# Optimization experiments

Measured on AMD Instinct MI355X. Metric: run time of the kernel, lower is better.

The kernel has to match this reference:

```python
import jax, jax.numpy as jnp
import numpy as np

D_MODEL = 1024
N_HEADS = 16
HEAD_DIM = D_MODEL // N_HEADS


def setup_inputs() -> dict:
    key = jax.random.key(0)
    ks = jax.random.split(key, 11)
    B, S = 2, 2048
    s = 1.0 / np.sqrt(D_MODEL)
    return {
        "query": jax.random.normal(ks[0], (B, S, D_MODEL), jnp.float32),
        "key": jax.random.normal(ks[1], (B, S, D_MODEL), jnp.float32),
        "value": jax.random.normal(ks[2], (B, S, D_MODEL), jnp.float32),
        "Wq": jax.random.normal(ks[3], (D_MODEL, D_MODEL), jnp.float32) * s,
        "bq": jnp.zeros((D_MODEL,), jnp.float32),
        "Wk": jax.random.normal(ks[4], (D_MODEL, D_MODEL), jnp.float32) * s,
        "bk": jnp.zeros((D_MODEL,), jnp.float32),
        "Wv": jax.random.normal(ks[5], (D_MODEL, D_MODEL), jnp.float32) * s,
        "bv": jnp.zeros((D_MODEL,), jnp.float32),
        "Wo": jax.random.normal(ks[6], (D_MODEL, D_MODEL), jnp.float32) * s,
        "bo": jnp.zeros((D_MODEL,), jnp.float32),
    }


def reference(query, key, value, Wq, bq, Wk, bk, Wv, bv, Wo, bo):
    B, S, _ = query.shape
    H, Dh = N_HEADS, HEAD_DIM
    scale = jnp.sqrt(jnp.asarray(Dh, query.dtype))
    # projections (torch Linear: x @ W.T + b)
    Q = (query @ Wq.T + bq).reshape(B, S, H, Dh).transpose(0, 2, 1, 3)  # [B,H,S,Dh]
    K = (key @ Wk.T + bk).reshape(B, S, H, Dh).transpose(0, 2, 1, 3)
    V = (value @ Wv.T + bv).reshape(B, S, H, Dh).transpose(0, 2, 1, 3)
    # full score matrix, matching the naive formulation
    energy = jnp.einsum("bhqd,bhkd->bhqk", Q, K) / scale  # [B,H,S,S]
    attn = jax.nn.softmax(energy, axis=-1)
    # dropout: eval mode -> identity
    out = jnp.einsum("bhqk,bhkd->bhqd", attn, V)  # [B,H,S,Dh]
    out = out.transpose(0, 2, 1, 3).reshape(B, S, H * Dh)
    return out @ Wo.T + bo
```

## Files before the change

### kernel.cpp

```cpp
#include <hip/hip_runtime.h>
#include <hip/hip_bf16.h>
#include <stdint.h>


typedef unsigned short u16;
typedef __attribute__((ext_vector_type(8))) short bf16x8;
typedef __attribute__((ext_vector_type(4))) float f32x4;

#define MFMA16 __builtin_amdgcn_mfma_f32_16x16x32_bf16
#define AS1 __attribute__((address_space(1)))
#define AS3 __attribute__((address_space(3)))

#define GM 4096
#define GN 1024
#define GK 1024
#define S_LEN 2048
#define NH 16
#define DH 64
#define KVBLK 64
#define PSTR 72

__device__ __forceinline__ u16 f2bf(float f) {
    union { float f; uint32_t u; } v; v.f = f;
    return (u16)((v.u + 0x7fffu + ((v.u >> 16) & 1u)) >> 16);
}

__device__ __forceinline__ uint32_t pack_bf16(float lo, float hi) {
    float2 t; t.x = lo; t.y = hi;
    __hip_bfloat162 h = __float22bfloat162_rn(t);
    return *(uint32_t*)&h;
}

__global__ __launch_bounds__(256) void cvt_all_kernel(
        const float* __restrict__ q, const float* __restrict__ k, const float* __restrict__ v,
        const float* __restrict__ Wq, const float* __restrict__ Wk,
        const float* __restrict__ Wv, const float* __restrict__ Wo,
        const float* __restrict__ bq,
        u16* __restrict__ qbf, u16* __restrict__ kbf, u16* __restrict__ vbf,
        u16* __restrict__ Wqb, u16* __restrict__ Wkb, u16* __restrict__ Wvb,
        u16* __restrict__ Wob, float* __restrict__ bqs, float qscale) {
    int bid = blockIdx.x;
    if (bid >= 8192) {
        int i = (bid - 8192) * 256 + (int)threadIdx.x;
        if (i < GN) bqs[i] = bq[i] * qscale;
        return;
    }
    const float* src; u16* dst; float scale = 1.f; int off;
    if      (bid < 2048) { src = q;  dst = qbf; off = bid; }
    else if (bid < 4096) { src = k;  dst = kbf; off = bid - 2048; }
    else if (bid < 6144) { src = v;  dst = vbf; off = bid - 4096; }
    else if (bid < 6656) { src = Wq; dst = Wqb; off = bid - 6144; scale = qscale; }
    else if (bid < 7168) { src = Wk; dst = Wkb; off = bid - 6656; }
    else if (bid < 7680) { src = Wv; dst = Wvb; off = bid - 7168; }
    else                 { src = Wo; dst = Wob; off = bid - 7680; }
    size_t i = (size_t)off * 256 + threadIdx.x;
    const f32x4* s = (const f32x4*)src + i * 2;
    f32x4 a = s[0], b = s[1];
    union { bf16x8 v8; u16 u[8]; } o;
    o.u[0] = f2bf(a[0] * scale); o.u[1] = f2bf(a[1] * scale);
    o.u[2] = f2bf(a[2] * scale); o.u[3] = f2bf(a[3] * scale);
    o.u[4] = f2bf(b[0] * scale); o.u[5] = f2bf(b[1] * scale);
    o.u[6] = f2bf(b[2] * scale); o.u[7] = f2bf(b[3] * scale);
    *(bf16x8*)(dst + i * 8) = o.v8;
}

template<int BK>
__device__ __forceinline__ void gemm_core(const u16* __restrict__ A,
                                          const u16* __restrict__ W,
                                          const float* __restrict__ bias,
                                          void* __restrict__ Cout, int mode,
                                          u16* As, u16* Bs,
                                          int mbase, int nbase) {
    const int t  = threadIdx.x;
    const int l  = t & 63;
    const int w  = t >> 6;
    const int wr = w >> 1, wc = w & 1;
    const int cl = l & 15, g = l >> 4;
    constexpr int CPR  = BK / 8;
    constexpr int NCH  = 128 * CPR / 256;
    constexpr int TE   = 128 * BK;

    f32x4 acc[4][4];
    f32x4 zero = {0.f, 0.f, 0.f, 0.f};
    #pragma unroll
    for (int i = 0; i < 4; ++i)
        #pragma unroll
        for (int j = 0; j < 4; ++j) acc[i][j] = zero;

    auto skey = [](int row) -> int {
        if constexpr (BK == 64) return row & 7;
        else                    return (row >> 1) & 3;
    };

    auto stage = [&](int buf, int kt) {
        #pragma unroll
        for (int r = 0; r < NCH; ++r) {
            int c = r * 256 + t;
            int row = c / CPR;
            int c8 = (c % CPR) ^ skey(row);
            __builtin_amdgcn_global_load_lds(
                (const AS1 void*)(A + (size_t)(mbase + row) * GK + kt + c8 * 8),
                (AS3 void*)(As + buf * TE + c * 8), 16, 0, 0);
            __builtin_amdgcn_global_load_lds(
                (const AS1 void*)(W + (size_t)(nbase + row) * GK + kt + c8 * 8),
                (AS3 void*)(Bs + buf * TE + c * 8), 16, 0, 0);
        }
    };

    stage(0, 0);
    __syncthreads();

    int cur = 0;
    for (int kt = 0; kt < GK; kt += BK) {
        if (kt + BK < GK) stage(cur ^ 1, kt + BK);

        const u16* Asb = As + cur * TE;
        const u16* Bsb = Bs + cur * TE;
        #pragma unroll
        for (int ks = 0; ks < BK / 32; ++ks) {
            bf16x8 af[4], bfr[4];
            #pragma unroll
            for (int mi = 0; mi < 4; ++mi) {
                int row = wr * 64 + mi * 16 + cl;
                af[mi] = *(const bf16x8*)&Asb[row * BK + ((ks * 4 + g) ^ skey(row)) * 8];
            }
            #pragma unroll
            for (int nj = 0; nj < 4; ++nj) {
                int row = wc * 64 + nj * 16 + cl;
                bfr[nj] = *(const bf16x8*)&Bsb[row * BK + ((ks * 4 + g) ^ skey(row)) * 8];
            }
            #pragma unroll
            for (int mi = 0; mi < 4; ++mi)
                #pragma unroll
                for (int nj = 0; nj < 4; ++nj)
                    acc[mi][nj] = MFMA16(af[mi], bfr[nj], acc[mi][nj], 0, 0, 0);
        }
        __syncthreads();
        cur ^= 1;
    }

    #pragma unroll
    for (int mi = 0; mi < 4; ++mi) {
        #pragma unroll
        for (int nj = 0; nj < 4; ++nj) {
            int n = nbase + wc * 64 + nj * 16 + cl;
            float bv = bias[n];
            #pragma unroll
            for (int r = 0; r < 4; ++r) {
                int m = mbase + wr * 64 + mi * 16 + g * 4 + r;
                float vv = acc[mi][nj][r] + bv;
                if (mode == 2) {
                    ((float*)Cout)[(size_t)m * GN + n] = vv;
                } else {
                    int b = m >> 11, s = m & 2047;
                    int hh = n >> 6, dh = n & 63;
                    if (mode == 0)
                        ((u16*)Cout)[(((size_t)(b * NH + hh)) * S_LEN + s) * DH + dh] = f2bf(vv);
                    else
                        ((u16*)Cout)[(((size_t)(b * NH + hh)) * DH + dh) * S_LEN + s] = f2bf(vv);
                }
            }
        }
    }
}

__global__ __launch_bounds__(256) void proj_gemm(
        const u16* __restrict__ qbf, const u16* __restrict__ kbf, const u16* __restrict__ vbf,
        const u16* __restrict__ Wqb, const u16* __restrict__ Wkb, const u16* __restrict__ Wvb,
        const float* __restrict__ bq, const float* __restrict__ bk, const float* __restrict__ bv,
        u16* __restrict__ Qb, u16* __restrict__ Kb, u16* __restrict__ Vtb) {
    __shared__ u16 As[2 * 128 * 32];
    __shared__ u16 Bs[2 * 128 * 32];
    int z = blockIdx.z;
    const u16* A   = (z == 0) ? qbf : (z == 1) ? kbf : vbf;
    const u16* W   = (z == 0) ? Wqb : (z == 1) ? Wkb : Wvb;
    const float* b = (z == 0) ? bq  : (z == 1) ? bk  : bv;
    u16* C         = (z == 0) ? Qb  : (z == 1) ? Kb  : Vtb;
    gemm_core<32>(A, W, b, (void*)C, (z == 2) ? 1 : 0, As, Bs,
                  blockIdx.y * 128, blockIdx.x * 128);
}

__global__ __launch_bounds__(256) void out_gemm(const u16* __restrict__ A,
                                                const u16* __restrict__ W,
                                                const float* __restrict__ bias,
                                                float* __restrict__ C) {
    __shared__ u16 As[2 * 128 * 64];
    __shared__ u16 Bs[2 * 128 * 64];
    int bid = blockIdx.x;
    int lid = (bid & 7) * 32 + (bid >> 3);
    int x = lid & 7, y = lid >> 3;
    gemm_core<64>(A, W, bias, (void*)C, 2, As, Bs, y * 128, x * 128);
}

__global__ __launch_bounds__(512, 4) void attn_kernel(const u16* __restrict__ Q,
                                                      const u16* __restrict__ Kb,
                                                      const u16* __restrict__ Vt,
                                                      u16* __restrict__ O) {
    __shared__ u16 Ks[3][KVBLK * 64];
    __shared__ u16 Vs[3][KVBLK * 64];
    __shared__ u16 Pl[8][16 * PSTR];

    const int t = threadIdx.x, l = t & 63, w = t >> 6;
    const int cl = l & 15, g = l >> 4;
    const int bh = blockIdx.x;
    const int b = bh >> 4, h = bh & 15;
    const int qw = blockIdx.y * 128 + w * 16;

    const u16* Qp = Q  + ((size_t)bh * S_LEN + qw) * DH;
    const u16* Kp = Kb + (size_t)bh * S_LEN * DH;
    const u16* Vp = Vt + (size_t)bh * DH * S_LEN;

    bf16x8 qf0 = *(const bf16x8*)(Qp + (size_t)cl * DH + g * 8);
    bf16x8 qf1 = *(const bf16x8*)(Qp + (size_t)cl * DH + 32 + g * 8);

    float rs = 0.f;
    f32x4 oacc[4];
    f32x4 zero = {0.f, 0.f, 0.f, 0.f};
    #pragma unroll
    for (int tt = 0; tt < 4; ++tt) oacc[tt] = zero;

    u16* P = Pl[w];

    const int srow = t >> 3;
    const int sc8  = (t & 7) ^ (srow & 7);
    const u16* Kg = Kp + (size_t)srow * DH + sc8 * 8;
    const u16* Vg = Vp + (size_t)srow * S_LEN + sc8 * 8;

    #define STAGE(buf, kvoff)                                                            \
        do {                                                                             \
            __builtin_amdgcn_global_load_lds(                                            \
                (const AS1 void*)(Kg + (size_t)(kvoff) * DH),                            \
                (AS3 void*)(&Ks[buf][0] + t * 8), 16, 0, 0);                             \
            __builtin_amdgcn_global_load_lds(                                            \
                (const AS1 void*)(Vg + (kvoff)),                                         \
                (AS3 void*)(&Vs[buf][0] + t * 8), 16, 0, 0);                             \
        } while (0)

    STAGE(0, 0);
    STAGE(1, KVBLK);
    asm volatile("s_waitcnt vmcnt(2)" ::: "memory");
    __builtin_amdgcn_s_barrier();

    const int NT = S_LEN / KVBLK;
    int cur = 0;
    for (int it = 0; it < NT; ++it) {
        if (it + 2 < NT) {
            int nb = cur + 2; if (nb >= 3) nb -= 3;
            STAGE(nb, (it + 2) * KVBLK);
        }

        const u16* Ksb = &Ks[cur][0];
        const u16* Vsb = &Vs[cur][0];

        f32x4 s[4];
        #pragma unroll
        for (int j = 0; j < 4; ++j) s[j] = zero;
        __builtin_amdgcn_s_setprio(1);
        #pragma unroll
        for (int j = 0; j < 4; ++j) {
            int row = j * 16 + cl, rx = row & 7;
            bf16x8 k0 = *(const bf16x8*)&Ksb[row * 64 + ((g)     ^ rx) * 8];
            bf16x8 k1 = *(const bf16x8*)&Ksb[row * 64 + ((4 + g) ^ rx) * 8];
            s[j] = MFMA16(k0, qf0, s[j], 0, 0, 0);
            s[j] = MFMA16(k1, qf1, s[j], 0, 0, 0);
        }
        __builtin_amdgcn_s_setprio(0);

        #pragma unroll
        for (int j = 0; j < 4; ++j) {
            float p0 = __builtin_amdgcn_exp2f(s[j][0]);
            float p1 = __builtin_amdgcn_exp2f(s[j][1]);
            float p2 = __builtin_amdgcn_exp2f(s[j][2]);
            float p3 = __builtin_amdgcn_exp2f(s[j][3]);
            rs += (p0 + p1) + (p2 + p3);
            uint2 pk;
            pk.x = pack_bf16(p0, p1);
            pk.y = pack_bf16(p2, p3);
            *(uint2*)&P[cl * PSTR + j * 16 + g * 4] = pk;
        }

        bf16x8 pf[2];
        #pragma unroll
        for (int ks = 0; ks < 2; ++ks)
            pf[ks] = *(const bf16x8*)&P[cl * PSTR + ks * 32 + g * 8];

        __builtin_amdgcn_s_setprio(1);
        #pragma unroll
        for (int tt = 0; tt < 4; ++tt) {
            int row = tt * 16 + cl, rx = row & 7;
            #pragma unroll
            for (int ks = 0; ks < 2; ++ks) {
                bf16x8 vf = *(const bf16x8*)&Vsb[row * 64 + ((ks * 4 + g) ^ rx) * 8];
                oacc[tt] = MFMA16(pf[ks], vf, oacc[tt], 0, 0, 0);
            }
        }
        __builtin_amdgcn_s_setprio(0);

        if (it + 2 < NT) {
            asm volatile("s_waitcnt vmcnt(2)\n\ts_barrier" ::: "memory");
        } else {
            asm volatile("s_waitcnt vmcnt(0)\n\ts_barrier" ::: "memory");
        }
        cur = (cur + 1 == 3) ? 0 : cur + 1;
    }
    #undef STAGE

    rs += __shfl_xor(rs, 16, 64);
    rs += __shfl_xor(rs, 32, 64);
    float rsq[4];
    #pragma unroll
    for (int r = 0; r < 4; ++r)
        rsq[r] = __shfl(rs, g * 4 + r, 64);

    #pragma unroll
    for (int tt = 0; tt < 4; ++tt) {
        #pragma unroll
        for (int r = 0; r < 4; ++r) {
            int q = qw + g * 4 + r;
            float val = oacc[tt][r] / rsq[r];
            O[((size_t)b * S_LEN + q) * GN + h * DH + tt * 16 + cl] = f2bf(val);
        }
    }
}

extern "C" void kernel_launch(void* const* d_in, const int* in_sizes, int n_in,
                              void* d_out, int out_size, void* d_ws, size_t ws_size,
                              hipStream_t stream) {
    const float* query = (const float*)d_in[0];
    const float* key   = (const float*)d_in[1];
    const float* value = (const float*)d_in[2];
    const float* Wq = (const float*)d_in[3];
    const float* bq = (const float*)d_in[4];
    const float* Wk = (const float*)d_in[5];
    const float* bk = (const float*)d_in[6];
    const float* Wv = (const float*)d_in[7];
    const float* bv = (const float*)d_in[8];
    const float* Wo = (const float*)d_in[9];
    const float* bo = (const float*)d_in[10];
    float* out = (float*)d_out;

    const float QSCALE = 0.125f * 1.4426950408889634f;

    u16* ws = (u16*)d_ws;
    const size_t MD = (size_t)GM * GN;
    const size_t WW = (size_t)GN * GK;
    u16* qbf = ws;
    u16* kbf = qbf + MD;
    u16* vbf = kbf + MD;
    u16* Wqb = vbf + MD;
    u16* Wkb = Wqb + WW;
    u16* Wvb = Wkb + WW;
    u16* Wob = Wvb + WW;
    u16* Qb  = Wob + WW;
    u16* Kbf = Qb  + MD;
    u16* Vtb = Kbf + MD;
    u16* Ob  = Vtb + MD;
    float* bqs = (float*)(Ob + MD);

    cvt_all_kernel<<<8196, 256, 0, stream>>>(query, key, value, Wq, Wk, Wv, Wo, bq,
                                             qbf, kbf, vbf, Wqb, Wkb, Wvb, Wob,
                                             bqs, QSCALE);

    dim3 gproj(GN / 128, GM / 128, 3);
    proj_gemm<<<gproj, 256, 0, stream>>>(qbf, kbf, vbf, Wqb, Wkb, Wvb,
                                         bqs, bk, bv, Qb, Kbf, Vtb);

    dim3 gattn(2 * NH, S_LEN / 128);
    attn_kernel<<<gattn, 512, 0, stream>>>(Qb, Kbf, Vtb, Ob);

    out_gemm<<<256, 256, 0, stream>>>(Ob, Wob, bo, out);
}
```

Before: 126.4 us.

## Software-pipeline attention QK^T one tile ahead and shrink out-GEMM K tile

The attention loop is restructured so the QK^T MFMAs for the next KV tile are issued before the exp/PV work of the current tile, with ping-pong score registers and K loads staged three tiles ahead and V two tiles ahead. The aim is to overlap the exp2 and LDS traffic of the softmax with matrix-core work and deepen the load pipeline. Separately, the output GEMM switches from a K-tile of 64 to 32, halving its shared memory, which may allow more resident blocks at the cost of more loop iterations. The extra live score registers may raise VGPR pressure under the 512x4 launch bound.

```diff
diff --git a/kernel.cpp b/kernel.cpp
--- a/kernel.cpp
+++ b/kernel.cpp
@@ -184,12 +184,12 @@
                                                 const u16* __restrict__ W,
                                                 const float* __restrict__ bias,
                                                 float* __restrict__ C) {
-    __shared__ u16 As[2 * 128 * 64];
-    __shared__ u16 Bs[2 * 128 * 64];
+    __shared__ u16 As[2 * 128 * 32];
+    __shared__ u16 Bs[2 * 128 * 32];
     int bid = blockIdx.x;
     int lid = (bid & 7) * 32 + (bid >> 3);
     int x = lid & 7, y = lid >> 3;
-    gemm_core<64>(A, W, bias, (void*)C, 2, As, Bs, y * 128, x * 128);
+    gemm_core<32>(A, W, bias, (void*)C, 2, As, Bs, y * 128, x * 128);
 }
 
 __global__ __launch_bounds__(512, 4) void attn_kernel(const u16* __restrict__ Q,
@@ -220,90 +220,110 @@
     for (int tt = 0; tt < 4; ++tt) oacc[tt] = zero;
 
     u16* P = Pl[w];
+    const int NT = S_LEN / KVBLK;
 
     const int srow = t >> 3;
     const int sc8  = (t & 7) ^ (srow & 7);
     const u16* Kg = Kp + (size_t)srow * DH + sc8 * 8;
     const u16* Vg = Vp + (size_t)srow * S_LEN + sc8 * 8;
 
-    #define STAGE(buf, kvoff)                                                            \
-        do {                                                                             \
-            __builtin_amdgcn_global_load_lds(                                            \
-                (const AS1 void*)(Kg + (size_t)(kvoff) * DH),                            \
-                (AS3 void*)(&Ks[buf][0] + t * 8), 16, 0, 0);                             \
-            __builtin_amdgcn_global_load_lds(                                            \
-                (const AS1 void*)(Vg + (kvoff)),                                         \
-                (AS3 void*)(&Vs[buf][0] + t * 8), 16, 0, 0);                             \
-        } while (0)
-
-    STAGE(0, 0);
-    STAGE(1, KVBLK);
+    #define STAGE_K(buf, kvoff)                                                   \
+        __builtin_amdgcn_global_load_lds(                                         \
+            (const AS1 void*)(Kg + (size_t)(kvoff) * DH),                         \
+            (AS3 void*)(&Ks[buf][0] + t * 8), 16, 0, 0)
+    #define STAGE_V(buf, kvoff)                                                   \
+        __builtin_amdgcn_global_load_lds(                                         \
+            (const AS1 void*)(Vg + (kvoff)),                                      \
+            (AS3 void*)(&Vs[buf][0] + t * 8), 16, 0, 0)
+
+    STAGE_K(0, 0);
+    STAGE_K(1, KVBLK);
+    STAGE_V(0, 0);
+    STAGE_K(2, 2 * KVBLK);
+    STAGE_V(1, KVBLK);
     asm volatile("s_waitcnt vmcnt(2)" ::: "memory");
     __builtin_amdgcn_s_barrier();
 
-    const int NT = S_LEN / KVBLK;
-    int cur = 0;
-    for (int it = 0; it < NT; ++it) {
-        if (it + 2 < NT) {
-            int nb = cur + 2; if (nb >= 3) nb -= 3;
-            STAGE(nb, (it + 2) * KVBLK);
-        }
-
-        const u16* Ksb = &Ks[cur][0];
-        const u16* Vsb = &Vs[cur][0];
-
-        f32x4 s[4];
-        #pragma unroll
-        for (int j = 0; j < 4; ++j) s[j] = zero;
-        __builtin_amdgcn_s_setprio(1);
+    f32x4 sA[4], sB[4];
+    {
+        const u16* Kn = &Ks[0][0];
         #pragma unroll
         for (int j = 0; j < 4; ++j) {
-            int row = j * 16 + cl, rx = row & 7;
-            bf16x8 k0 = *(const bf16x8*)&Ksb[row * 64 + ((g)     ^ rx) * 8];
-            bf16x8 k1 = *(const bf16x8*)&Ksb[row * 64 + ((4 + g) ^ rx) * 8];
-            s[j] = MFMA16(k0, qf0, s[j], 0, 0, 0);
-            s[j] = MFMA16(k1, qf1, s[j], 0, 0, 0);
-        }
-        __builtin_amdgcn_s_setprio(0);
-
-        #pragma unroll
-        for (int j = 0; j < 4; ++j) {
-            float p0 = __builtin_amdgcn_exp2f(s[j][0]);
-            float p1 = __builtin_amdgcn_exp2f(s[j][1]);
-            float p2 = __builtin_amdgcn_exp2f(s[j][2]);
-            float p3 = __builtin_amdgcn_exp2f(s[j][3]);
-            rs += (p0 + p1) + (p2 + p3);
-            uint2 pk;
-            pk.x = pack_bf16(p0, p1);
-            pk.y = pack_bf16(p2, p3);
-            *(uint2*)&P[cl * PSTR + j * 16 + g * 4] = pk;
-        }
-
-        bf16x8 pf[2];
-        #pragma unroll
-        for (int ks = 0; ks < 2; ++ks)
-            pf[ks] = *(const bf16x8*)&P[cl * PSTR + ks * 32 + g * 8];
-
-        __builtin_amdgcn_s_setprio(1);
-        #pragma unroll
-        for (int tt = 0; tt < 4; ++tt) {
-            int row = tt * 16 + cl, rx = row & 7;
-            #pragma unroll
-            for (int ks = 0; ks < 2; ++ks) {
-                bf16x8 vf = *(const bf16x8*)&Vsb[row * 64 + ((ks * 4 + g) ^ rx) * 8];
-                oacc[tt] = MFMA16(pf[ks], vf, oacc[tt], 0, 0, 0);
-            }
-        }
-        __builtin_amdgcn_s_setprio(0);
-
-        if (it + 2 < NT) {
-            asm volatile("s_waitcnt vmcnt(2)\n\ts_barrier" ::: "memory");
-        } else {
-            asm volatile("s_waitcnt vmcnt(0)\n\ts_barrier" ::: "memory");
-        }
-        cur = (cur + 1 == 3) ? 0 : cur + 1;
-    }
-    #undef STAGE
+            int row = j * 16 + cl, rxx = row & 7;
+            bf16x8 k0 = *(const bf16x8*)&Kn[row * 64 + ((g)     ^ rxx) * 8];
+            bf16x8 k1 = *(const bf16x8*)&Kn[row * 64 + ((4 + g) ^ rxx) * 8];
+            f32x4 tmp = zero;
+            tmp   = MFMA16(k0, qf0, tmp, 0, 0, 0);
+            sA[j] = MFMA16(k1, qf1, tmp, 0, 0, 0);
+        }
+    }
+    __builtin_amdgcn_s_barrier();
+
+    #define ATT_ITER(IT, SC, SN)                                                       \
+    {                                                                                  \
+        const int it_ = (IT);                                                          \
+        const int cur_ = it_ % 3;                                                      \
+        const int nx1_ = (it_ + 1) % 3;                                                \
+        const int nx2_ = (it_ + 2) % 3;                                                \
+        if (it_ + 3 < NT) STAGE_K(cur_, (it_ + 3) * KVBLK);                            \
+        if (it_ + 2 < NT) STAGE_V(nx2_, (it_ + 2) * KVBLK);                            \
+        if (it_ + 1 < NT) {                                                            \
+            const u16* Kn = &Ks[nx1_][0];                                              \
+            __builtin_amdgcn_s_setprio(1);                                             \
+            _Pragma("unroll")                                                          \
+            for (int j = 0; j < 4; ++j) {                                              \
+                int row = j * 16 + cl, rxx = row & 7;                                  \
+                bf16x8 k0 = *(const bf16x8*)&Kn[row * 64 + ((g)     ^ rxx) * 8];       \
+                bf16x8 k1 = *(const bf16x8*)&Kn[row * 64 + ((4 + g) ^ rxx) * 8];       \
+                f32x4 tmp = zero;                                                      \
+                tmp   = MFMA16(k0, qf0, tmp, 0, 0, 0);                                 \
+                SN[j] = MFMA16(k1, qf1, tmp, 0, 0, 0);                                 \
+            }                                                                          \
+            __builtin_amdgcn_s_setprio(0);                                             \
+        }                                                                              \
+        _Pragma("unroll")                                                              \
+        for (int j = 0; j < 4; ++j) {                                                  \
+            float p0 = __builtin_amdgcn_exp2f(SC[j][0]);                               \
+            float p1 = __builtin_amdgcn_exp2f(SC[j][1]);                               \
+            float p2 = __builtin_amdgcn_exp2f(SC[j][2]);                               \
+            float p3 = __builtin_amdgcn_exp2f(SC[j][3]);                               \
+            rs += (p0 + p1) + (p2 + p3);                                               \
+            uint2 pk;                                                                  \
+            pk.x = pack_bf16(p0, p1);                                                  \
+            pk.y = pack_bf16(p2, p3);                                                  \
+            *(uint2*)&P[cl * PSTR + j * 16 + g * 4] = pk;                              \
+        }                                                                              \
+        {                                                                              \
+            bf16x8 pf0 = *(const bf16x8*)&P[cl * PSTR + g * 8];                        \
+            bf16x8 pf1 = *(const bf16x8*)&P[cl * PSTR + 32 + g * 8];                   \
+            const u16* Vc = &Vs[cur_][0];                                              \
+            __builtin_amdgcn_s_setprio(1);                                             \
+            _Pragma("unroll")                                                          \
+            for (int tt = 0; tt < 4; ++tt) {                                           \
+                int row = tt * 16 + cl, rxx = row & 7;                                 \
+                bf16x8 vf0 = *(const bf16x8*)&Vc[row * 64 + ((g)     ^ rxx) * 8];      \
+                bf16x8 vf1 = *(const bf16x8*)&Vc[row * 64 + ((4 + g) ^ rxx) * 8];      \
+                oacc[tt] = MFMA16(pf0, vf0, oacc[tt], 0, 0, 0);                        \
+                oacc[tt] = MFMA16(pf1, vf1, oacc[tt], 0, 0, 0);                        \
+            }                                                                          \
+            __builtin_amdgcn_s_setprio(0);                                             \
+        }                                                                              \
+        int nin_ = ((it_ + 3 < NT) ? 1 : 0) + ((it_ + 2 < NT) ? 1 : 0);                \
+        if (nin_ == 2)                                                                 \
+            asm volatile("s_waitcnt vmcnt(2)\n\ts_barrier" ::: "memory");              \
+        else if (nin_ == 1)                                                            \
+            asm volatile("s_waitcnt vmcnt(1)\n\ts_barrier" ::: "memory");              \
+        else                                                                           \
+            asm volatile("s_waitcnt vmcnt(0)\n\ts_barrier" ::: "memory");              \
+    }
+
+    for (int it = 0; it < NT; it += 2) {
+        ATT_ITER(it,     sA, sB);
+        ATT_ITER(it + 1, sB, sA);
+    }
+    #undef ATT_ITER
+    #undef STAGE_K
+    #undef STAGE_V
 
     rs += __shfl_xor(rs, 16, 64);
     rs += __shfl_xor(rs, 32, 64);
```

Measured after the change: 131.0 us. 3.7% more time.

## Keep softmax probabilities in registers by permuting K rows; shrink output GEMM K-tile

Applied to the files above, without the earlier changes.

The attention kernel reorders which K rows each lane's score MFMA covers, so the exp'd probabilities already sit in the register layout the PV MFMA wants. That removes the per-wave LDS round trip (store P, reload as fragments) and its buffer. The LDS swizzle for K/V staging and reads is rewritten to match the new row mapping. Separately, the output projection GEMM switches from a 64 to a 32 K-tile, halving its shared memory, which may improve occupancy at the cost of more loop iterations.

```diff
diff --git a/kernel.cpp b/kernel.cpp
--- a/kernel.cpp
+++ b/kernel.cpp
@@ -18,7 +18,6 @@
 #define NH 16
 #define DH 64
 #define KVBLK 64
-#define PSTR 72
 
 __device__ __forceinline__ u16 f2bf(float f) {
     union { float f; uint32_t u; } v; v.f = f;
@@ -184,12 +183,12 @@
                                                 const u16* __restrict__ W,
                                                 const float* __restrict__ bias,
                                                 float* __restrict__ C) {
-    __shared__ u16 As[2 * 128 * 64];
-    __shared__ u16 Bs[2 * 128 * 64];
+    __shared__ u16 As[2 * 128 * 32];
+    __shared__ u16 Bs[2 * 128 * 32];
     int bid = blockIdx.x;
     int lid = (bid & 7) * 32 + (bid >> 3);
     int x = lid & 7, y = lid >> 3;
-    gemm_core<64>(A, W, bias, (void*)C, 2, As, Bs, y * 128, x * 128);
+    gemm_core<32>(A, W, bias, (void*)C, 2, As, Bs, y * 128, x * 128);
 }
 
 __global__ __launch_bounds__(512, 4) void attn_kernel(const u16* __restrict__ Q,
@@ -198,7 +197,6 @@
                                                       u16* __restrict__ O) {
     __shared__ u16 Ks[3][KVBLK * 64];
     __shared__ u16 Vs[3][KVBLK * 64];
-    __shared__ u16 Pl[8][16 * PSTR];
 
     const int t = threadIdx.x, l = t & 63, w = t >> 6;
     const int cl = l & 15, g = l >> 4;
@@ -219,10 +217,11 @@
     #pragma unroll
     for (int tt = 0; tt < 4; ++tt) oacc[tt] = zero;
 
-    u16* P = Pl[w];
+    const int kx = (cl & 3) | (((cl >> 2) & 1) << 2);
+    const int vx = (cl & 3) | (((cl >> 3) & 1) << 2);
 
     const int srow = t >> 3;
-    const int sc8  = (t & 7) ^ (srow & 7);
+    const int sc8  = (t & 7) ^ ((srow & 3) | (((srow >> 3) & 1) << 2));
     const u16* Kg = Kp + (size_t)srow * DH + sc8 * 8;
     const u16* Vg = Vp + (size_t)srow * S_LEN + sc8 * 8;
 
@@ -258,39 +257,41 @@
         __builtin_amdgcn_s_setprio(1);
         #pragma unroll
         for (int j = 0; j < 4; ++j) {
-            int row = j * 16 + cl, rx = row & 7;
-            bf16x8 k0 = *(const bf16x8*)&Ksb[row * 64 + ((g)     ^ rx) * 8];
-            bf16x8 k1 = *(const bf16x8*)&Ksb[row * 64 + ((4 + g) ^ rx) * 8];
+            int row = ((j & 1) << 5) + ((cl >> 2) << 3) + ((j >> 1) << 2) + (cl & 3);
+            bf16x8 k0 = *(const bf16x8*)&Ksb[row * 64 + ((g)     ^ kx) * 8];
+            bf16x8 k1 = *(const bf16x8*)&Ksb[row * 64 + ((4 + g) ^ kx) * 8];
             s[j] = MFMA16(k0, qf0, s[j], 0, 0, 0);
             s[j] = MFMA16(k1, qf1, s[j], 0, 0, 0);
         }
         __builtin_amdgcn_s_setprio(0);
 
+        float p[4][4];
         #pragma unroll
         for (int j = 0; j < 4; ++j) {
-            float p0 = __builtin_amdgcn_exp2f(s[j][0]);
-            float p1 = __builtin_amdgcn_exp2f(s[j][1]);
-            float p2 = __builtin_amdgcn_exp2f(s[j][2]);
-            float p3 = __builtin_amdgcn_exp2f(s[j][3]);
-            rs += (p0 + p1) + (p2 + p3);
-            uint2 pk;
-            pk.x = pack_bf16(p0, p1);
-            pk.y = pack_bf16(p2, p3);
-            *(uint2*)&P[cl * PSTR + j * 16 + g * 4] = pk;
-        }
-
+            p[j][0] = __builtin_amdgcn_exp2f(s[j][0]);
+            p[j][1] = __builtin_amdgcn_exp2f(s[j][1]);
+            p[j][2] = __builtin_amdgcn_exp2f(s[j][2]);
+            p[j][3] = __builtin_amdgcn_exp2f(s[j][3]);
+            rs += (p[j][0] + p[j][1]) + (p[j][2] + p[j][3]);
+        }
         bf16x8 pf[2];
         #pragma unroll
-        for (int ks = 0; ks < 2; ++ks)
-            pf[ks] = *(const bf16x8*)&P[cl * PSTR + ks * 32 + g * 8];
+        for (int ks = 0; ks < 2; ++ks) {
+            union { bf16x8 v8; uint32_t u[4]; } pk;
+            pk.u[0] = pack_bf16(p[ks][0],     p[ks][1]);
+            pk.u[1] = pack_bf16(p[ks][2],     p[ks][3]);
+            pk.u[2] = pack_bf16(p[ks + 2][0], p[ks + 2][1]);
+            pk.u[3] = pack_bf16(p[ks + 2][2], p[ks + 2][3]);
+            pf[ks] = pk.v8;
+        }
 
         __builtin_amdgcn_s_setprio(1);
         #pragma unroll
         for (int tt = 0; tt < 4; ++tt) {
-            int row = tt * 16 + cl, rx = row & 7;
+            int row = tt * 16 + cl;
             #pragma unroll
             for (int ks = 0; ks < 2; ++ks) {
-                bf16x8 vf = *(const bf16x8*)&Vsb[row * 64 + ((ks * 4 + g) ^ rx) * 8];
+                bf16x8 vf = *(const bf16x8*)&Vsb[row * 64 + ((ks * 4 + g) ^ vx) * 8];
                 oacc[tt] = MFMA16(pf[ks], vf, oacc[tt], 0, 0, 0);
             }
         }
```

Result: no change. 125.8 us (-0.5%).
